# Kernel tuning notes

Hardware: AMD Instinct MI355X
Metric: run time of the kernel (lower is better)

The kernel has to match this reference:

```python
import jax, jax.numpy as jnp
import numpy as np

VOCAB, EMBED, HIDDEN = 32000, 512, 1024
B, T = 32, 512


def setup_inputs() -> dict:
    key = jax.random.key(0)
    k1, k2, k3, k4, k5, k6 = jax.random.split(key, 6)
    s_ih = 1.0 / np.sqrt(HIDDEN)
    return {
        "input_ids": jax.random.randint(k1, (B, T), 0, VOCAB, dtype=jnp.int32),
        "h0": jax.random.normal(k2, (1, B, HIDDEN), dtype=jnp.float32),
        "c0": jax.random.normal(k3, (1, B, HIDDEN), dtype=jnp.float32),
        "emb": jax.random.normal(k4, (VOCAB, EMBED), dtype=jnp.float32),
        # PyTorch LSTM weights: weight_ih [4H, E], weight_hh [4H, H], gate order i,f,g,o; bias=False
        "W_ih": jax.random.uniform(k5, (4 * HIDDEN, EMBED), dtype=jnp.float32, minval=-s_ih, maxval=s_ih),
        "W_hh": jax.random.uniform(k6, (4 * HIDDEN, HIDDEN), dtype=jnp.float32, minval=-s_ih, maxval=s_ih),
    }


def _lstm(x, h0, c0, W_ih, W_hh):
    # x: [B,T,E]; precompute input projections once (the only big GEMM)
    x_proj = jnp.einsum("bte,ge->tbg", x, W_ih)  # [T,B,4H]
    H = W_hh.shape[1]

    def step(carry, xt):
        h, c = carry
        gates = xt + h @ W_hh.T  # [B,4H]
        i, f, g, o = jnp.split(gates, 4, axis=-1)
        c = jax.nn.sigmoid(f) * c + jax.nn.sigmoid(i) * jnp.tanh(g)
        h = jax.nn.sigmoid(o) * jnp.tanh(c)
        return (h, c), h

    (hn, cn), ys = jax.lax.scan(step, (h0, c0), x_proj)
    return jnp.transpose(ys, (1, 0, 2)), hn, cn  # output [B,T,H]


def reference(input_ids, h0, c0, emb, W_ih, W_hh):
    embedded = emb[input_ids]  # [B,T,E] embedding lookup
    output, hn, cn = _lstm(embedded, h0[0], c0[0], W_ih, W_hh)
    return output, hn[None], cn[None]
```

## Files before the change

### kernel.cpp

```cpp
#include <hip/hip_runtime.h>
#include <hip/hip_bf16.h>
#include <hip/hip_cooperative_groups.h>

#define E   512
#define H   1024
#define BB  32
#define TT  512
#define G4  4096
#define NBLK 64
#define YS_ELEMS 16777216

typedef __attribute__((ext_vector_type(8))) short bf16x8;
typedef __attribute__((ext_vector_type(4))) float f32x4;

__device__ __forceinline__ unsigned short f2bf(float x){
    union { float f; unsigned u; } v; v.f = x;
    unsigned r = v.u + 0x7fffu + ((v.u >> 16) & 1u);
    return (unsigned short)(r >> 16);
}
__device__ __forceinline__ float bf2f(unsigned short b){
    union { unsigned u; float f; } v; v.u = ((unsigned)b) << 16;
    return v.f;
}
__device__ __forceinline__ float sigm(float x){ return 1.f/(1.f+__expf(-x)); }
__device__ __forceinline__ float tanh_(float x){ return 2.f/(1.f+__expf(-2.f*x)) - 1.f; }

__global__ void k_prep(const int* __restrict__ ids, const float* __restrict__ emb,
                       const float* __restrict__ Wih, const float* __restrict__ Whh,
                       const float* __restrict__ h0,
                       unsigned short* __restrict__ Abf, unsigned short* __restrict__ Bbf,
                       unsigned short* __restrict__ Wb,  unsigned short* __restrict__ hb,
                       unsigned* __restrict__ flags)
{
    int bx = blockIdx.x, tx = threadIdx.x;
    if (bx == 0) flags[tx] = 0;
    const float* src; unsigned short* dst;
    if (bx < 4096) {
        unsigned u = bx*256u + tx;
        int m  = u >> 6;
        int e0 = (u & 63) * 8;
        int row = ids[(m & 31) * TT + (m >> 5)];
        src = emb + (size_t)row * E + e0;
        dst = Abf + (size_t)m   * E + e0;
    } else if (bx < 5120) {
        size_t off = ((size_t)(bx-4096)*256u + tx) * 8;
        src = Wih + off; dst = Bbf + off;
    } else if (bx < 7168) {
        size_t off = ((size_t)(bx-5120)*256u + tx) * 8;
        src = Whh + off; dst = Wb + off;
    } else {
        size_t off = ((size_t)(bx-7168)*256u + tx) * 8;
        src = h0 + off; dst = hb + off;
    }
    float4 f0 = *(const float4*)(src);
    float4 f1 = *(const float4*)(src + 4);
    uint4 o;
    o.x = f2bf(f0.x) | ((unsigned)f2bf(f0.y) << 16);
    o.y = f2bf(f0.z) | ((unsigned)f2bf(f0.w) << 16);
    o.z = f2bf(f1.x) | ((unsigned)f2bf(f1.y) << 16);
    o.w = f2bf(f1.z) | ((unsigned)f2bf(f1.w) << 16);
    *(uint4*)dst = o;
}

__global__ __launch_bounds__(256) void k_gemm(const unsigned short* __restrict__ A,
        const unsigned short* __restrict__ Bm, unsigned short* __restrict__ C)
{
    __shared__ __align__(16) unsigned short As[128][40];
    __shared__ __align__(16) unsigned short Bs[128][40];
    int tid = threadIdx.x;
    int bm = blockIdx.x & 127;
    int bn = blockIdx.x >> 7;
    int w = tid >> 6, lane = tid & 63, l15 = lane & 15, quad = lane >> 4;
    int wm = w & 1, wn = w >> 1;
    f32x4 acc[4][4] = {};
    for (int kt = 0; kt < 16; ++kt) {
        __syncthreads();
        for (int i = 0; i < 2; ++i) {
            int c = tid + 256*i;
            int row = c >> 2, kc = (c & 3) * 8;
            *(uint4*)&As[row][kc] = *(const uint4*)(A  + ((size_t)(bm*128 + row))*E + kt*32 + kc);
            *(uint4*)&Bs[row][kc] = *(const uint4*)(Bm + ((size_t)(bn*128 + row))*E + kt*32 + kc);
        }
        __syncthreads();
        bf16x8 af[4], bfr[4];
        for (int i = 0; i < 4; ++i) af[i]  = *(const bf16x8*)&As[wm*64 + i*16 + l15][quad*8];
        for (int j = 0; j < 4; ++j) bfr[j] = *(const bf16x8*)&Bs[wn*64 + j*16 + l15][quad*8];
        for (int i = 0; i < 4; ++i)
            for (int j = 0; j < 4; ++j)
                acc[i][j] = __builtin_amdgcn_mfma_f32_16x16x32_bf16(af[i], bfr[j], acc[i][j], 0,0,0);
    }
    for (int i = 0; i < 4; ++i)
        for (int j = 0; j < 4; ++j)
            for (int r = 0; r < 4; ++r) {
                int mg = bm*128 + wm*64 + i*16 + quad*4 + r;
                int ng = bn*128 + wn*64 + j*16 + l15;
                C[(size_t)mg * G4 + ng] = f2bf(acc[i][j][r]);
            }
}

__global__ __launch_bounds__(512, 1) void k_recur(const unsigned short* __restrict__ xp,
        const unsigned short* __restrict__ Wb, unsigned short* __restrict__ hbuf,
        const float* __restrict__ c0, float* __restrict__ out,
        unsigned* __restrict__ flags)
{
    __shared__ __align__(16) unsigned short Hs[BB*H];
    __shared__ __align__(16) float gbuf[4][32][66];
    int tid = threadIdx.x;
    int blk = blockIdx.x;
    int w = tid >> 6, lane = tid & 63, l15 = lane & 15, quad = lane >> 4;
    int nh = w >> 2, kq = w & 3;

    bf16x8 wf0[8], wf1[8];
    {
        const unsigned short* wp0 = Wb + (size_t)((nh*2+0)*H + blk*16 + l15)*H + kq*256 + quad*8;
        const unsigned short* wp1 = wp0 + (size_t)H*H;
#define WLD(d, p, O) asm volatile("global_load_dwordx4 %0, %1, off offset:" O \
                                  : "=v"(d) : "v"(p))
        WLD(wf0[0], wp0, "0");   WLD(wf0[1], wp0, "64");
        WLD(wf0[2], wp0, "128"); WLD(wf0[3], wp0, "192");
        WLD(wf0[4], wp0, "256"); WLD(wf0[5], wp0, "320");
        WLD(wf0[6], wp0, "384"); WLD(wf0[7], wp0, "448");
        WLD(wf1[0], wp1, "0");   WLD(wf1[1], wp1, "64");
        WLD(wf1[2], wp1, "128"); WLD(wf1[3], wp1, "192");
        WLD(wf1[4], wp1, "256"); WLD(wf1[5], wp1, "320");
        WLD(wf1[6], wp1, "384"); WLD(wf1[7], wp1, "448");
#undef WLD
        asm volatile("s_waitcnt vmcnt(0)" ::: "memory");
        __builtin_amdgcn_sched_barrier(0);
    }
    int b   = lane & 31;
    int kp  = lane >> 5;
    int cl0 = (w & 3)*4 + kp*2;
    int kg0 = blk*16 + cl0;
    float cA = 0.f, cB = 0.f;
    if (tid < 256) {
        float2 cc = *(const float2*)(c0 + b*H + kg0);
        cA = cc.x; cB = cc.y;
    }

    unsigned inrow = (unsigned)(tid & 127) * 16;
    unsigned rhi   = (unsigned)tid >> 7;
    char* dw_e = (char*)Hs + rhi*2048 + (inrow ^ (rhi << 4));
    char* dw_o = (char*)Hs + rhi*2048 + ((inrow ^ (rhi << 4)) ^ 64u);
    const char* g0 = (const char*)hbuf + (size_t)tid*16;
    const char* g1 = g0 + BB*H*2;

    const char* hsb = (const char*)Hs;
    unsigned abase = (unsigned)kq*512u + (((unsigned)(l15 >> 2) & 1u)*64u)
                   + ((unsigned)(quad ^ (l15 & 3))*16u);
    const char* pe0 = hsb + l15*2048 + abase;
    const char* po0 = hsb + l15*2048 + (abase ^ 64u);
    const char* pe1 = pe0 + 16*2048;
    const char* po1 = po0 + 16*2048;

    __syncthreads();

    for (int t = 0; t < TT; ++t) {
        if (tid < 64) {
            unsigned tgt = (unsigned)t;
            const unsigned* fp = flags + lane;
            bool ok;
            do {
                unsigned f0 = __hip_atomic_load(fp,       __ATOMIC_RELAXED, __HIP_MEMORY_SCOPE_AGENT);
                unsigned f1 = __hip_atomic_load(fp + 64,  __ATOMIC_RELAXED, __HIP_MEMORY_SCOPE_AGENT);
                unsigned f2 = __hip_atomic_load(fp + 128, __ATOMIC_RELAXED, __HIP_MEMORY_SCOPE_AGENT);
                unsigned f3 = __hip_atomic_load(fp + 192, __ATOMIC_RELAXED, __HIP_MEMORY_SCOPE_AGENT);
                ok = (f0 >= tgt) & (f1 >= tgt) & (f2 >= tgt) & (f3 >= tgt);
            } while (!__all(ok));
        }
        __syncthreads();
        const char* gsel = (t & 1) ? g1 : g0;
        uint4 s0,s1,s2,s3,s4,s5,s6,s7;
#define SLD(d,i) asm volatile("global_load_dwordx4 %0, %1, off sc0 sc1" \
                              : "=v"(d) : "v"(gsel + (size_t)(i)*8192))
        SLD(s0,0); SLD(s1,1); SLD(s2,2); SLD(s3,3);
        SLD(s4,4); SLD(s5,5); SLD(s6,6); SLD(s7,7);
#undef SLD
        unsigned xw0, xw1, xw2, xw3;
        if (tid < 256) {
            const char* xb0 = (const char*)(xp + ((size_t)t*BB + b)*G4 + kg0);
            const char* xb1 = xb0 + 4096;
            asm volatile("global_load_dword %0, %1, off"             : "=v"(xw0) : "v"(xb0));
            asm volatile("global_load_dword %0, %1, off offset:2048" : "=v"(xw1) : "v"(xb0));
            asm volatile("global_load_dword %0, %1, off"             : "=v"(xw2) : "v"(xb1));
            asm volatile("global_load_dword %0, %1, off offset:2048" : "=v"(xw3) : "v"(xb1));
            asm volatile("s_waitcnt vmcnt(4)" ::: "memory");
        } else {
            asm volatile("s_waitcnt vmcnt(0)" ::: "memory");
        }
        __builtin_amdgcn_sched_barrier(0);
        *(uint4*)(dw_e +     0) = s0;  *(uint4*)(dw_o +  8192) = s1;
        *(uint4*)(dw_e + 16384) = s2;  *(uint4*)(dw_o + 24576) = s3;
        *(uint4*)(dw_e + 32768) = s4;  *(uint4*)(dw_o + 40960) = s5;
        *(uint4*)(dw_e + 49152) = s6;  *(uint4*)(dw_o + 57344) = s7;
        __syncthreads();
        f32x4 a00 = {}, a01 = {}, a10 = {}, a11 = {};
        #pragma unroll
        for (int k2 = 0; k2 < 8; ++k2) {
            const char* q0 = (k2 & 1) ? po0 : pe0;
            const char* q1 = (k2 & 1) ? po1 : pe1;
            bf16x8 A0 = *(const bf16x8*)(q0 + (k2 >> 1)*128);
            bf16x8 A1 = *(const bf16x8*)(q1 + (k2 >> 1)*128);
            a00 = __builtin_amdgcn_mfma_f32_16x16x32_bf16(A0, wf0[k2], a00, 0,0,0);
            a10 = __builtin_amdgcn_mfma_f32_16x16x32_bf16(A1, wf0[k2], a10, 0,0,0);
            a01 = __builtin_amdgcn_mfma_f32_16x16x32_bf16(A0, wf1[k2], a01, 0,0,0);
            a11 = __builtin_amdgcn_mfma_f32_16x16x32_bf16(A1, wf1[k2], a11, 0,0,0);
        }
        {
            int n0 = nh*32 + l15, n1 = n0 + 16;
            #pragma unroll
            for (int r = 0; r < 4; ++r) {
                gbuf[kq][quad*4 + r][n0]      = a00[r];
                gbuf[kq][quad*4 + r][n1]      = a01[r];
                gbuf[kq][16 + quad*4 + r][n0] = a10[r];
                gbuf[kq][16 + quad*4 + r][n1] = a11[r];
            }
        }
        __syncthreads();
        if (tid < 256) {
            asm volatile("s_waitcnt vmcnt(0)" ::: "memory");
            __builtin_amdgcn_sched_barrier(0);
            float xA[4], xB[4];
            xA[0] = bf2f((unsigned short)(xw0 & 0xffffu)); xB[0] = bf2f((unsigned short)(xw0 >> 16));
            xA[1] = bf2f((unsigned short)(xw1 & 0xffffu)); xB[1] = bf2f((unsigned short)(xw1 >> 16));
            xA[2] = bf2f((unsigned short)(xw2 & 0xffffu)); xB[2] = bf2f((unsigned short)(xw2 >> 16));
            xA[3] = bf2f((unsigned short)(xw3 & 0xffffu)); xB[3] = bf2f((unsigned short)(xw3 >> 16));
            float pA[4], pB[4];
            #pragma unroll
            for (int g = 0; g < 4; ++g) {
                float2 s = *(const float2*)&gbuf[0][b][g*16 + cl0];
                float2 u = *(const float2*)&gbuf[1][b][g*16 + cl0];
                float2 v = *(const float2*)&gbuf[2][b][g*16 + cl0];
                float2 z = *(const float2*)&gbuf[3][b][g*16 + cl0];
                pA[g] = ((s.x + u.x) + (v.x + z.x)) + xA[g];
                pB[g] = ((s.y + u.y) + (v.y + z.y)) + xB[g];
            }
            float iA = sigm(pA[0]), fA = sigm(pA[1]), gA = tanh_(pA[2]), oA = sigm(pA[3]);
            float iB = sigm(pB[0]), fB = sigm(pB[1]), gB = tanh_(pB[2]), oB = sigm(pB[3]);
            cA = fA * cA + iA * gA;
            cB = fB * cB + iB * gB;
            float hA = oA * tanh_(cA);
            float hB = oB * tanh_(cB);
            unsigned short* nxt = hbuf + ((t+1) & 1) * (BB*H);
            unsigned hp = (unsigned)f2bf(hA) | ((unsigned)f2bf(hB) << 16);
            __hip_atomic_store((unsigned*)(nxt + b*H + kg0), hp,
                               __ATOMIC_RELAXED, __HIP_MEMORY_SCOPE_AGENT);
            asm volatile("s_waitcnt vmcnt(0)" ::: "memory");
            if (lane == 0)
                __hip_atomic_store(&flags[w*64 + blk], (unsigned)(t+1),
                                   __ATOMIC_RELAXED, __HIP_MEMORY_SCOPE_AGENT);
            *(float2*)(out + (size_t)b*(TT*H) + (size_t)t*H + kg0) = make_float2(hA, hB);
            if (t == TT-1) {
                *(float2*)(out + YS_ELEMS + b*H + kg0)         = make_float2(hA, hB);
                *(float2*)(out + YS_ELEMS + 32768 + b*H + kg0) = make_float2(cA, cB);
            }
        }
    }
}

extern "C" void kernel_launch(void* const* d_in, const int* in_sizes, int n_in,
                              void* d_out, int out_size, void* d_ws, size_t ws_size,
                              hipStream_t stream)
{
    const int*   ids = (const int*)  d_in[0];
    const float* h0  = (const float*)d_in[1];
    const float* c0  = (const float*)d_in[2];
    const float* emb = (const float*)d_in[3];
    const float* Wih = (const float*)d_in[4];
    const float* Whh = (const float*)d_in[5];
    float* out = (float*)d_out;
    char* ws = (char*)d_ws;
    unsigned short* xp  = (unsigned short*)(ws);
    unsigned short* Abf = (unsigned short*)(ws + 134217728);
    unsigned short* Bbf = (unsigned short*)(ws + 134217728 + 16777216);
    unsigned short* Wb  = (unsigned short*)(ws + 134217728 + 16777216 + 4194304);
    unsigned short* hb  = (unsigned short*)(ws + 134217728 + 16777216 + 4194304 + 8388608);
    unsigned*       fl  = (unsigned*)      (ws + 134217728 + 16777216 + 4194304 + 8388608 + 131072);

    k_prep<<<7184, 256, 0, stream>>>(ids, emb, Wih, Whh, h0, Abf, Bbf, Wb, hb, fl);
    k_gemm<<<4096, 256, 0, stream>>>(Abf, Bbf, xp);
    void* args[] = { (void*)&xp, (void*)&Wb, (void*)&hb, (void*)&c0, (void*)&out, (void*)&fl };
    hipLaunchCooperativeKernel((void*)k_recur, dim3(NBLK), dim3(512), args, 0, stream);
}
```

Before: 3.431 ms.

## Replace global barrier with per-chunk flag waits and direct global h loads

Drops the LDS staging of the hidden state. Each wave now loads its h fragments straight from global memory into MFMA operands and pipelines the loads with the MFMAs. Instead of one wave spinning on every producer's flags before a block barrier, each wave waits only on the two producer blocks that own the k-chunk it is about to consume. Each block now publishes a single flag after an extra block barrier rather than one flag per wave. The aim is to overlap inter-block synchronisation with compute and cut LDS traffic, at the cost of more global loads, extra spin traffic and one more barrier per step.

```diff
diff --git a/kernel.cpp b/kernel.cpp
--- a/kernel.cpp
+++ b/kernel.cpp
@@ -103,7 +103,6 @@
         const float* __restrict__ c0, float* __restrict__ out,
         unsigned* __restrict__ flags)
 {
-    __shared__ __align__(16) unsigned short Hs[BB*H];
     __shared__ __align__(16) float gbuf[4][32][66];
     int tid = threadIdx.x;
     int blk = blockIdx.x;
@@ -138,44 +137,13 @@
         cA = cc.x; cB = cc.y;
     }
 
-    unsigned inrow = (unsigned)(tid & 127) * 16;
-    unsigned rhi   = (unsigned)tid >> 7;
-    char* dw_e = (char*)Hs + rhi*2048 + (inrow ^ (rhi << 4));
-    char* dw_o = (char*)Hs + rhi*2048 + ((inrow ^ (rhi << 4)) ^ 64u);
-    const char* g0 = (const char*)hbuf + (size_t)tid*16;
-    const char* g1 = g0 + BB*H*2;
-
-    const char* hsb = (const char*)Hs;
-    unsigned abase = (unsigned)kq*512u + (((unsigned)(l15 >> 2) & 1u)*64u)
-                   + ((unsigned)(quad ^ (l15 & 3))*16u);
-    const char* pe0 = hsb + l15*2048 + abase;
-    const char* po0 = hsb + l15*2048 + (abase ^ 64u);
-    const char* pe1 = pe0 + 16*2048;
-    const char* po1 = po0 + 16*2048;
-
+    const char* hb0 = (const char*)hbuf + ((size_t)l15*H + (size_t)kq*256 + (size_t)quad*8)*2;
     __syncthreads();
 
     for (int t = 0; t < TT; ++t) {
-        if (tid < 64) {
-            unsigned tgt = (unsigned)t;
-            const unsigned* fp = flags + lane;
-            bool ok;
-            do {
-                unsigned f0 = __hip_atomic_load(fp,       __ATOMIC_RELAXED, __HIP_MEMORY_SCOPE_AGENT);
-                unsigned f1 = __hip_atomic_load(fp + 64,  __ATOMIC_RELAXED, __HIP_MEMORY_SCOPE_AGENT);
-                unsigned f2 = __hip_atomic_load(fp + 128, __ATOMIC_RELAXED, __HIP_MEMORY_SCOPE_AGENT);
-                unsigned f3 = __hip_atomic_load(fp + 192, __ATOMIC_RELAXED, __HIP_MEMORY_SCOPE_AGENT);
-                ok = (f0 >= tgt) & (f1 >= tgt) & (f2 >= tgt) & (f3 >= tgt);
-            } while (!__all(ok));
-        }
-        __syncthreads();
-        const char* gsel = (t & 1) ? g1 : g0;
-        uint4 s0,s1,s2,s3,s4,s5,s6,s7;
-#define SLD(d,i) asm volatile("global_load_dwordx4 %0, %1, off sc0 sc1" \
-                              : "=v"(d) : "v"(gsel + (size_t)(i)*8192))
-        SLD(s0,0); SLD(s1,1); SLD(s2,2); SLD(s3,3);
-        SLD(s4,4); SLD(s5,5); SLD(s6,6); SLD(s7,7);
-#undef SLD
+        unsigned tgt = (unsigned)t;
+        const char* pa0 = hb0 + ((t & 1) ? 65536 : 0);
+        const char* pa1 = pa0 + 32768;
         unsigned xw0, xw1, xw2, xw3;
         if (tid < 256) {
             const char* xb0 = (const char*)(xp + ((size_t)t*BB + b)*G4 + kg0);
@@ -184,39 +152,52 @@
             asm volatile("global_load_dword %0, %1, off offset:2048" : "=v"(xw1) : "v"(xb0));
             asm volatile("global_load_dword %0, %1, off"             : "=v"(xw2) : "v"(xb1));
             asm volatile("global_load_dword %0, %1, off offset:2048" : "=v"(xw3) : "v"(xb1));
-            asm volatile("s_waitcnt vmcnt(4)" ::: "memory");
-        } else {
-            asm volatile("s_waitcnt vmcnt(0)" ::: "memory");
-        }
-        __builtin_amdgcn_sched_barrier(0);
-        *(uint4*)(dw_e +     0) = s0;  *(uint4*)(dw_o +  8192) = s1;
-        *(uint4*)(dw_e + 16384) = s2;  *(uint4*)(dw_o + 24576) = s3;
-        *(uint4*)(dw_e + 32768) = s4;  *(uint4*)(dw_o + 40960) = s5;
-        *(uint4*)(dw_e + 49152) = s6;  *(uint4*)(dw_o + 57344) = s7;
-        __syncthreads();
-        f32x4 a00 = {}, a01 = {}, a10 = {}, a11 = {};
-        #pragma unroll
-        for (int k2 = 0; k2 < 8; ++k2) {
-            const char* q0 = (k2 & 1) ? po0 : pe0;
-            const char* q1 = (k2 & 1) ? po1 : pe1;
-            bf16x8 A0 = *(const bf16x8*)(q0 + (k2 >> 1)*128);
-            bf16x8 A1 = *(const bf16x8*)(q1 + (k2 >> 1)*128);
-            a00 = __builtin_amdgcn_mfma_f32_16x16x32_bf16(A0, wf0[k2], a00, 0,0,0);
-            a10 = __builtin_amdgcn_mfma_f32_16x16x32_bf16(A1, wf0[k2], a10, 0,0,0);
-            a01 = __builtin_amdgcn_mfma_f32_16x16x32_bf16(A0, wf1[k2], a01, 0,0,0);
-            a11 = __builtin_amdgcn_mfma_f32_16x16x32_bf16(A1, wf1[k2], a11, 0,0,0);
-        }
+        }
+        f32x4 acc00 = {}, acc01 = {}, acc10 = {}, acc11 = {};
+        bf16x8 a0A, a1A, a0B, a1B;
+#define SPIN(P) { const unsigned* fp_ = flags + (kq*16 + 2*(P) + (lane & 1)); \
+                  unsigned f_ = __hip_atomic_load(fp_, __ATOMIC_RELAXED, __HIP_MEMORY_SCOPE_AGENT); \
+                  while (!__all(f_ >= tgt)) { \
+                      __builtin_amdgcn_s_sleep(1); \
+                      f_ = __hip_atomic_load(fp_, __ATOMIC_RELAXED, __HIP_MEMORY_SCOPE_AGENT); \
+                  } }
+#define ISSUE(S, O) \
+        asm volatile("global_load_dwordx4 %0, %1, off offset:" O " sc0 sc1" : "=v"(a0##S) : "v"(pa0)); \
+        asm volatile("global_load_dwordx4 %0, %1, off offset:" O " sc0 sc1" : "=v"(a1##S) : "v"(pa1));
+#define WAIT2 asm volatile("s_waitcnt vmcnt(2)" ::: "memory"); __builtin_amdgcn_sched_barrier(0);
+#define WAIT0 asm volatile("s_waitcnt vmcnt(0)" ::: "memory"); __builtin_amdgcn_sched_barrier(0);
+#define MFMA4(S, P) \
+        acc00 = __builtin_amdgcn_mfma_f32_16x16x32_bf16(a0##S, wf0[P], acc00, 0,0,0); \
+        acc10 = __builtin_amdgcn_mfma_f32_16x16x32_bf16(a1##S, wf0[P], acc10, 0,0,0); \
+        acc01 = __builtin_amdgcn_mfma_f32_16x16x32_bf16(a0##S, wf1[P], acc01, 0,0,0); \
+        acc11 = __builtin_amdgcn_mfma_f32_16x16x32_bf16(a1##S, wf1[P], acc11, 0,0,0);
+
+        SPIN(0) ISSUE(A, "0")
+        SPIN(1) ISSUE(B, "64")  WAIT2 MFMA4(A, 0)
+        SPIN(2) ISSUE(A, "128") WAIT2 MFMA4(B, 1)
+        SPIN(3) ISSUE(B, "192") WAIT2 MFMA4(A, 2)
+        SPIN(4) ISSUE(A, "256") WAIT2 MFMA4(B, 3)
+        SPIN(5) ISSUE(B, "320") WAIT2 MFMA4(A, 4)
+        SPIN(6) ISSUE(A, "384") WAIT2 MFMA4(B, 5)
+        SPIN(7) ISSUE(B, "448") WAIT2 MFMA4(A, 6)
+        WAIT0 MFMA4(B, 7)
+#undef SPIN
+#undef ISSUE
+#undef WAIT2
+#undef WAIT0
+#undef MFMA4
         {
             int n0 = nh*32 + l15, n1 = n0 + 16;
             #pragma unroll
             for (int r = 0; r < 4; ++r) {
-                gbuf[kq][quad*4 + r][n0]      = a00[r];
-                gbuf[kq][quad*4 + r][n1]      = a01[r];
-                gbuf[kq][16 + quad*4 + r][n0] = a10[r];
-                gbuf[kq][16 + quad*4 + r][n1] = a11[r];
-            }
-        }
-        __syncthreads();
+                gbuf[kq][quad*4 + r][n0]      = acc00[r];
+                gbuf[kq][quad*4 + r][n1]      = acc01[r];
+                gbuf[kq][16 + quad*4 + r][n0] = acc10[r];
+                gbuf[kq][16 + quad*4 + r][n1] = acc11[r];
+            }
+        }
+        __syncthreads();
+        float hA = 0.f, hB = 0.f;
         if (tid < 256) {
             asm volatile("s_waitcnt vmcnt(0)" ::: "memory");
             __builtin_amdgcn_sched_barrier(0);
@@ -239,16 +220,19 @@
             float iB = sigm(pB[0]), fB = sigm(pB[1]), gB = tanh_(pB[2]), oB = sigm(pB[3]);
             cA = fA * cA + iA * gA;
             cB = fB * cB + iB * gB;
-            float hA = oA * tanh_(cA);
-            float hB = oB * tanh_(cB);
+            hA = oA * tanh_(cA);
+            hB = oB * tanh_(cB);
             unsigned short* nxt = hbuf + ((t+1) & 1) * (BB*H);
             unsigned hp = (unsigned)f2bf(hA) | ((unsigned)f2bf(hB) << 16);
             __hip_atomic_store((unsigned*)(nxt + b*H + kg0), hp,
                                __ATOMIC_RELAXED, __HIP_MEMORY_SCOPE_AGENT);
             asm volatile("s_waitcnt vmcnt(0)" ::: "memory");
-            if (lane == 0)
-                __hip_atomic_store(&flags[w*64 + blk], (unsigned)(t+1),
-                                   __ATOMIC_RELAXED, __HIP_MEMORY_SCOPE_AGENT);
+        }
+        __syncthreads();
+        if (tid == 0)
+            __hip_atomic_store(&flags[blk], (unsigned)(t+1),
+                               __ATOMIC_RELAXED, __HIP_MEMORY_SCOPE_AGENT);
+        if (tid < 256) {
             *(float2*)(out + (size_t)b*(TT*H) + (size_t)t*H + kg0) = make_float2(hA, hB);
             if (t == TT-1) {
                 *(float2*)(out + YS_ELEMS + b*H + kg0)         = make_float2(hA, hB);
```

Measured after the change: 3.841 ms. +11.9%, slower.
